# Optimization experiments

Hardware: AMD Instinct MI355X
Metric: run time of the kernel (lower is better)

Reference implementation:

```python
import jax, jax.numpy as jnp
import numpy as np

EPS_LN = 1e-05   # LayerNorm eps in SimpleCogVideoXLayerNormZero
EPS_QK = 1e-06   # RMSNorm eps for qk_norm

DIM = 2048
FFN = 8192
HEADS = 16
HEAD_DIM = DIM // HEADS
TEMB = 512
F, H, W = 4, 24, 24
SEQ = F * H * W  # 2304
B = 1


def _layernorm(x, weight, bias, eps):
    mu = jnp.mean(x, axis=-1, keepdims=True)
    var = jnp.mean((x - mu) ** 2, axis=-1, keepdims=True)
    return (x - mu) * jax.lax.rsqrt(var + eps) * weight + bias


def _rmsnorm(x, weight, eps):
    var = jnp.mean(x * x, axis=-1, keepdims=True)
    return x * jax.lax.rsqrt(var + eps) * weight


def _ln_zero(x, temb, lin_w, lin_b, n_w, n_b):
    # shift/scale/gate modulation from temb
    t = jax.nn.silu(temb) @ lin_w + lin_b          # [B, 3*dim]
    shift, scale, gate = jnp.split(t, 3, axis=1)
    xn = _layernorm(x, n_w, n_b, EPS_LN)
    return xn * (1.0 + scale)[:, None, :] + shift[:, None, :], gate[:, None, :]


def _rope(x, cos, sin):
    # x: [B, S, H, D]; cos/sin: [S, 1, D] broadcastable
    x1 = x[..., 0::2]
    x2 = x[..., 1::2]
    c = cos[..., 0::2]
    s = sin[..., 1::2]
    even = x1 * c - x2 * s
    odd = x1 * s + x2 * c
    return jnp.stack([even, odd], axis=-1).reshape(x.shape)


def _forward(hidden_states, ref_states, temb, cos_h, sin_h, cos_r, sin_r,
             ln1_lw, ln1_lb, ln1_nw, ln1_nb, ln2_lw, ln2_lb, ln2_nw, ln2_nb,
             wq, bq, wk, bk, wv, bv, nq_w, nk_w, wo, bo,
             ffn_w1, ffn_b1, ffn_w2, ffn_b2, f, h, w):
    b, s, dim = hidden_states.shape
    heads = HEADS
    hd = dim // heads
    scale = hd ** -0.5

    def qkv(x, cos, sin):
        q = _rmsnorm(x @ wq + bq, nq_w, EPS_QK)
        k = _rmsnorm(x @ wk + bk, nk_w, EPS_QK)
        v = x @ wv + bv
        q = q.reshape(b, s, heads, hd)
        k = k.reshape(b, s, heads, hd)
        v = v.reshape(b, s, heads, hd)
        q = _rope(q, cos, sin)
        k = _rope(k, cos, sin)
        return q, k, v

    def attn(nh, nr):
        q, k, v = qkv(nh, cos_h, sin_h)
        rq, rk, rv = qkv(nr, cos_r, sin_r)

        def combine(a, ra):
            a = a.reshape(b, f, h, w, heads, hd)
            ra = ra.reshape(b, f, h, w, heads, hd)
            c = jnp.concatenate([a, ra], axis=3)          # [b,f,h,2w,H,D]
            return c.reshape(b * f, h * 2 * w, heads, hd)  # [(bf),(h 2w),H,D]

        cq, ck, cv = combine(q, rq), combine(k, rk), combine(v, rv)
        logits = jnp.einsum('bqhd,bkhd->bhqk', cq, ck) * scale
        probs = jax.nn.softmax(logits, axis=-1)
        out = jnp.einsum('bhqk,bkhd->bqhd', probs, cv)
        out = out.reshape(b, f, h, 2 * w, heads, hd)
        ah = out[:, :, :, :w].reshape(b, s, dim)
        ar = out[:, :, :, w:].reshape(b, s, dim)
        return ah @ wo + bo, ar @ wo + bo

    def ffn(x):
        return jax.nn.gelu(x @ ffn_w1 + ffn_b1, approximate=True) @ ffn_w2 + ffn_b2

    norm_h, gate_h = _ln_zero(hidden_states, temb, ln1_lw, ln1_lb, ln1_nw, ln1_nb)
    norm_r, gate_r = _ln_zero(ref_states, temb, ln1_lw, ln1_lb, ln1_nw, ln1_nb)
    attn_h, attn_r = attn(norm_h, norm_r)

    hidden_states = hidden_states + gate_h * attn_h
    norm_h2, gate_ff = _ln_zero(hidden_states, temb, ln2_lw, ln2_lb, ln2_nw, ln2_nb)
    ref_states = ref_states + gate_r * attn_r
    norm_r2, gate_ff_r = _ln_zero(ref_states, temb, ln2_lw, ln2_lb, ln2_nw, ln2_nb)

    hidden_states = hidden_states + gate_ff * ffn(norm_h2)
    ref_states = ref_states + gate_ff_r * ffn(norm_r2)
    return hidden_states, ref_states


def setup_inputs() -> dict:
    key = jax.random.key(0)
    ks = jax.random.split(key, 24)
    std = 0.02
    inp = {
        'hidden_states': jax.random.normal(ks[0], (B, SEQ, DIM), jnp.float32),
        'ref_states': jax.random.normal(ks[1], (B, SEQ, DIM), jnp.float32),
        'temb': jax.random.normal(ks[2], (B, TEMB), jnp.float32),
        'cos_h': jax.random.uniform(ks[3], (SEQ, 1, HEAD_DIM), jnp.float32),
        'sin_h': jax.random.uniform(ks[4], (SEQ, 1, HEAD_DIM), jnp.float32),
        'cos_r': jax.random.uniform(ks[5], (SEQ, 1, HEAD_DIM), jnp.float32),
        'sin_r': jax.random.uniform(ks[6], (SEQ, 1, HEAD_DIM), jnp.float32),
        'ln1_lw': jax.random.normal(ks[7], (TEMB, 3 * DIM), jnp.float32) * std,
        'ln1_lb': jnp.zeros((3 * DIM,), jnp.float32),
        'ln1_nw': jnp.ones((DIM,), jnp.float32),
        'ln1_nb': jnp.zeros((DIM,), jnp.float32),
        'ln2_lw': jax.random.normal(ks[8], (TEMB, 3 * DIM), jnp.float32) * std,
        'ln2_lb': jnp.zeros((3 * DIM,), jnp.float32),
        'ln2_nw': jnp.ones((DIM,), jnp.float32),
        'ln2_nb': jnp.zeros((DIM,), jnp.float32),
        'wq': jax.random.normal(ks[9], (DIM, DIM), jnp.float32) * std,
        'bq': jnp.zeros((DIM,), jnp.float32),
        'wk': jax.random.normal(ks[10], (DIM, DIM), jnp.float32) * std,
        'bk': jnp.zeros((DIM,), jnp.float32),
        'wv': jax.random.normal(ks[11], (DIM, DIM), jnp.float32) * std,
        'bv': jnp.zeros((DIM,), jnp.float32),
        'nq_w': jnp.ones((DIM,), jnp.float32),
        'nk_w': jnp.ones((DIM,), jnp.float32),
        'wo': jax.random.normal(ks[12], (DIM, DIM), jnp.float32) * std,
        'bo': jnp.zeros((DIM,), jnp.float32),
        'ffn_w1': jax.random.normal(ks[13], (DIM, FFN), jnp.float32) * std,
        'ffn_b1': jnp.zeros((FFN,), jnp.float32),
        'ffn_w2': jax.random.normal(ks[14], (FFN, DIM), jnp.float32) * std,
        'ffn_b2': jnp.zeros((DIM,), jnp.float32),
        'f': F, 'h': H, 'w': W,
    }
    return inp


def reference(hidden_states, ref_states, temb, cos_h, sin_h, cos_r, sin_r,
              ln1_lw, ln1_lb, ln1_nw, ln1_nb, ln2_lw, ln2_lb, ln2_nw, ln2_nb,
              wq, bq, wk, bk, wv, bv, nq_w, nk_w, wo, bo,
              ffn_w1, ffn_b1, ffn_w2, ffn_b2, f, h, w):
    return _forward(hidden_states, ref_states, temb, cos_h, sin_h, cos_r, sin_r,
                    ln1_lw, ln1_lb, ln1_nw, ln1_nb, ln2_lw, ln2_lb, ln2_nw, ln2_nb,
                    wq, bq, wk, bk, wv, bv, nq_w, nk_w, wo, bo,
                    ffn_w1, ffn_b1, ffn_w2, ffn_b2, f, h, w)
```

## Files before the change

### kernel.cpp

```cpp
#include <hip/hip_runtime.h>

typedef unsigned int u32;
typedef unsigned short us16;
typedef __bf16 bf16x8 __attribute__((ext_vector_type(8)));
typedef float f32x4 __attribute__((ext_vector_type(4)));

constexpr int S    = 2304;
constexpr int S2   = 4608;
constexpr int D    = 2048;
constexpr int NQKV = 3 * D;
constexpr int NH   = 16;
constexpr int HD   = 128;
constexpr int FFN  = 8192;
constexpr int CT   = 1152;
constexpr float ATTN_SCALE = 0.08838834764831845f;

__device__ __forceinline__ us16 f2bf(float f) {
  u32 x = __float_as_uint(f);
  x += 0x7fffu + ((x >> 16) & 1u);
  return (us16)(x >> 16);
}
__device__ __forceinline__ float blk_sum256(float v, float* red, int tid) {
  #pragma unroll
  for (int o = 32; o; o >>= 1) v += __shfl_down(v, o, 64);
  __syncthreads();
  if ((tid & 63) == 0) red[tid >> 6] = v;
  __syncthreads();
  return red[0] + red[1] + red[2] + red[3];
}

typedef const __attribute__((address_space(1))) void* gas_ptr;
typedef __attribute__((address_space(3))) void* las_ptr;
__device__ __forceinline__ void gload16(const us16* g, us16* l) {
  __builtin_amdgcn_global_load_lds((gas_ptr)g, (las_ptr)l, 16, 0, 0);
}

__device__ __forceinline__ float gelu_tanh(float x) {
  float y = 0.7978845608028654f * (x + 0.044715f * x * x * x);
  float e = __expf(2.0f * y);
  float t = 1.0f - 2.0f / (e + 1.0f);
  return 0.5f * x * (1.0f + t);
}

__global__ __launch_bounds__(256) void transpose_cvt(
    const float* __restrict__ in, us16* __restrict__ out, int Kd, int Nd) {
  __shared__ float tile[32][33];
  int tx = threadIdx.x, ty = threadIdx.y;
  int n0 = blockIdx.x * 32, k0 = blockIdx.y * 32;
  #pragma unroll
  for (int i = 0; i < 4; i++)
    tile[ty + i * 8][tx] = in[(size_t)(k0 + ty + i * 8) * Nd + n0 + tx];
  __syncthreads();
  #pragma unroll
  for (int i = 0; i < 4; i++)
    out[(size_t)(n0 + ty + i * 8) * Kd + k0 + tx] = f2bf(tile[tx][ty + i * 8]);
}

__global__ __launch_bounds__(256) void temb_mod(
    const float* __restrict__ temb,
    const float* __restrict__ lw1, const float* __restrict__ lb1,
    const float* __restrict__ lw2, const float* __restrict__ lb2,
    float* __restrict__ t1, float* __restrict__ t2) {
  __shared__ float st[512];
  int tid = threadIdx.x;
  for (int i = tid; i < 512; i += 256) {
    float v = temb[i];
    st[i] = v / (1.0f + __expf(-v));
  }
  __syncthreads();
  int which = blockIdx.x / 24;
  int n = (blockIdx.x % 24) * 256 + tid;
  const float* lw = which ? lw2 : lw1;
  const float* lb = which ? lb2 : lb1;
  float acc = lb[n];
  #pragma unroll 4
  for (int k = 0; k < 512; k++) acc += st[k] * lw[(size_t)k * (3 * D) + n];
  (which ? t2 : t1)[n] = acc;
}

__global__ __launch_bounds__(256) void ln_mod(
    const float* __restrict__ x, const float* __restrict__ t,
    const float* __restrict__ nw, const float* __restrict__ nb,
    us16* __restrict__ out) {
  __shared__ float red[4];
  int tok = blockIdx.x, tid = threadIdx.x;
  const float* xr = x + (size_t)tok * D;
  float v[8];
  float4 a = *(const float4*)(xr + tid * 8);
  float4 b = *(const float4*)(xr + tid * 8 + 4);
  v[0]=a.x; v[1]=a.y; v[2]=a.z; v[3]=a.w; v[4]=b.x; v[5]=b.y; v[6]=b.z; v[7]=b.w;
  float s = 0;
  #pragma unroll
  for (int i = 0; i < 8; i++) s += v[i];
  float mu = blk_sum256(s, red, tid) * (1.0f / D);
  float sq = 0;
  #pragma unroll
  for (int i = 0; i < 8; i++) { float d = v[i] - mu; sq += d * d; }
  float var = blk_sum256(sq, red, tid) * (1.0f / D);
  float rinv = rsqrtf(var + 1e-5f);
  int n = tid * 8;
  us16 o[8];
  #pragma unroll
  for (int i = 0; i < 8; i++) {
    float xn = (v[i] - mu) * rinv * nw[n + i] + nb[n + i];
    float y = xn * (1.0f + t[D + n + i]) + t[n + i];
    o[i] = f2bf(y);
  }
  *(uint4*)(out + (size_t)tok * D + n) = *(uint4*)o;
}

template <int EPI>
__global__ __launch_bounds__(256) void gemm128(
    const us16* __restrict__ A, const us16* __restrict__ BT,
    const float* __restrict__ b0, const float* __restrict__ b1,
    const float* __restrict__ b2, int bmask, void* __restrict__ Cout,
    int M, int N, int K,
    const float* __restrict__ xa, const float* __restrict__ xb,
    const float* __restrict__ gate) {
  __shared__ __align__(16) us16 As[3][128 * 32];
  __shared__ __align__(16) us16 Bs[3][128 * 32];
  const int tid = threadIdx.x;

  const int nbx = N >> 7;
  const int nwg = nbx * (M >> 7);
  int bid = (int)blockIdx.x;
  bid = (bid & 7) * (nwg >> 3) + (bid >> 3);
  const int by = bid / nbx;
  const int m0 = by << 7;
  const int n0 = (bid - by * nbx) << 7;

  const int srow = tid >> 2;
  const int scol = (tid & 3) << 3;
  const us16* Ap = A + (size_t)(m0 + srow) * K + scol;
  const us16* Bp = BT + (size_t)(n0 + srow) * K + scol;
  const size_t rstep = (size_t)64 * K;
  const int wvofs = (tid >> 6) << 9;

  const int w = tid >> 6, l = tid & 63;
  const int wr = (w >> 1) << 6, wc = (w & 1) << 6;
  const int m = l & 15, quad = l >> 4;
  const int aoff = (wr + m) * 32 + quad * 8;
  const int boff = (wc + m) * 32 + quad * 8;

  us16 *p0a = &As[0][0], *p1a = &As[1][0], *p2a = &As[2][0];
  us16 *p0b = &Bs[0][0], *p1b = &Bs[1][0], *p2b = &Bs[2][0];

  gload16(Ap,          p0a + wvofs);
  gload16(Ap + rstep,  p0a + wvofs + 2048);
  gload16(Bp,          p0b + wvofs);
  gload16(Bp + rstep,  p0b + wvofs + 2048);
  gload16(Ap + 32,         p1a + wvofs);
  gload16(Ap + rstep + 32, p1a + wvofs + 2048);
  gload16(Bp + 32,         p1b + wvofs);
  gload16(Bp + rstep + 32, p1b + wvofs + 2048);
  asm volatile("s_waitcnt vmcnt(4)" ::: "memory");
  __builtin_amdgcn_s_barrier();
  __builtin_amdgcn_sched_barrier(0);

  f32x4 acc[4][4] = {};
  for (int k0 = 0; k0 < K; k0 += 32) {
    const int k2 = k0 + 64;
    if (k2 < K) {
      gload16(Ap + k2,         p2a + wvofs);
      gload16(Ap + rstep + k2, p2a + wvofs + 2048);
      gload16(Bp + k2,         p2b + wvofs);
      gload16(Bp + rstep + k2, p2b + wvofs + 2048);
    }
    __builtin_amdgcn_sched_barrier(0);
    bf16x8 af[4], bf[4];
    #pragma unroll
    for (int i = 0; i < 4; i++) {
      af[i] = *(const bf16x8*)(p0a + aoff + i * 512);
      bf[i] = *(const bf16x8*)(p0b + boff + i * 512);
    }
    #pragma unroll
    for (int mi = 0; mi < 4; mi++)
      #pragma unroll
      for (int ni = 0; ni < 4; ni++)
        acc[mi][ni] = __builtin_amdgcn_mfma_f32_16x16x32_bf16(
            af[mi], bf[ni], acc[mi][ni], 0, 0, 0);
    __builtin_amdgcn_sched_barrier(0);
    if (k2 < K) asm volatile("s_waitcnt vmcnt(4)" ::: "memory");
    else        asm volatile("s_waitcnt vmcnt(0)" ::: "memory");
    __builtin_amdgcn_s_barrier();
    __builtin_amdgcn_sched_barrier(0);
    us16* t;
    t = p0a; p0a = p1a; p1a = p2a; p2a = t;
    t = p0b; p0b = p1b; p1b = p2b; p2b = t;
  }

  const float* bp = b0;
  if (b1) { int seg = (n0 + wc) >> 11; if (seg == 1) bp = b1; else if (seg >= 2) bp = b2; }

  const int r0 = m0 + wr + (quad << 2);
  #pragma unroll
  for (int ni = 0; ni < 4; ni++) {
    const int col = n0 + wc + ni * 16 + m;
    const float bv = bp ? bp[col & bmask] : 0.0f;
    #pragma unroll
    for (int mi = 0; mi < 4; mi++) {
      const int row = r0 + mi * 16;
      #pragma unroll
      for (int r = 0; r < 4; r++) {
        float y = acc[mi][ni][r] + bv;
        if constexpr (EPI == 1) {
          ((us16*)Cout)[(size_t)(row + r) * N + col] = f2bf(gelu_tanh(y));
        } else if constexpr (EPI == 2) {
          const int rr = row + r;
          const float xv = (rr < S) ? xa[(size_t)rr * N + col]
                                    : xb[(size_t)(rr - S) * N + col];
          ((float*)Cout)[(size_t)rr * N + col] = xv + gate[col & bmask] * y;
        } else {
          ((float*)Cout)[(size_t)(row + r) * N + col] = y;
        }
      }
    }
  }
}

__global__ __launch_bounds__(256) void qkv_scatter(
    const float* __restrict__ raw,
    const float* __restrict__ nq_w, const float* __restrict__ nk_w,
    const float* __restrict__ cos_h, const float* __restrict__ sin_h,
    const float* __restrict__ cos_r, const float* __restrict__ sin_r,
    us16* __restrict__ qc, us16* __restrict__ kc, us16* __restrict__ vc) {
  __shared__ float red[4];
  int bid = blockIdx.x, tid = threadIdx.x;
  int mode = bid / S2;
  int t = bid - mode * S2;
  us16* out = mode == 0 ? qc : (mode == 1 ? kc : vc);
  const float* nw = mode == 1 ? nk_w : nq_w;
  int is_ref = t >= S;
  int tt = is_ref ? t - S : t;
  const float* xr = raw + (size_t)t * NQKV + mode * D;
  float v[8];
  float4 a = *(const float4*)(xr + tid * 8);
  float4 b = *(const float4*)(xr + tid * 8 + 4);
  v[0]=a.x; v[1]=a.y; v[2]=a.z; v[3]=a.w; v[4]=b.x; v[5]=b.y; v[6]=b.z; v[7]=b.w;
  int n = tid * 8;
  int head = n >> 7, d = n & 127;
  float o8[8];
  if (mode < 2) {
    float s = 0;
    #pragma unroll
    for (int i = 0; i < 8; i++) s += v[i] * v[i];
    float tot = blk_sum256(s, red, tid);
    float rinv = rsqrtf(tot * (1.0f / D) + 1e-6f);
    const float* cr = (is_ref ? cos_r : cos_h) + (size_t)tt * HD;
    const float* sr = (is_ref ? sin_r : sin_h) + (size_t)tt * HD;
    #pragma unroll
    for (int p = 0; p < 4; p++) {
      float x1 = v[2 * p] * rinv * nw[n + 2 * p];
      float x2 = v[2 * p + 1] * rinv * nw[n + 2 * p + 1];
      float ce = cr[d + 2 * p];
      float so = sr[d + 2 * p + 1];
      o8[2 * p]     = x1 * ce - x2 * so;
      o8[2 * p + 1] = x1 * so + x2 * ce;
    }
    if (mode == 0) {
      #pragma unroll
      for (int i = 0; i < 8; i++) o8[i] *= ATTN_SCALE;
    }
  } else {
    #pragma unroll
    for (int i = 0; i < 8; i++) o8[i] = v[i];
  }
  int f = tt / 576, rem = tt % 576;
  int row = rem / 24, col = rem - row * 24;
  int comb = row * 48 + col + (is_ref ? 24 : 0);
  size_t oidx = ((size_t)(f * NH + head) * CT + comb) * HD + d;
  us16 packed[8];
  #pragma unroll
  for (int i = 0; i < 8; i++) packed[i] = f2bf(o8[i]);
  *(uint4*)(out + oidx) = *(uint4*)packed;
}

__global__ __launch_bounds__(256) void attn_mfma(
    const us16* __restrict__ qc, const us16* __restrict__ kc,
    const us16* __restrict__ vc, us16* __restrict__ ah, us16* __restrict__ ar) {
  __shared__ __align__(16) us16 Qs[64][136];
  __shared__ __align__(16) us16 Ks[64][136];
  __shared__ __align__(16) us16 Vts[128][72];
  __shared__ __align__(16) us16 Ps[4][16][72];
  int tid = threadIdx.x;
  int w = tid >> 6, l = tid & 63;
  int m = l & 15, quad = l >> 4;
  int bx = blockIdx.x;
  int fh = bx / 18, qt = bx % 18;
  size_t base = (size_t)fh * CT * HD;
  int qbase = qt * 64;

  {
    int row = tid >> 2, c0 = (tid & 3) * 32;
    const us16* src = qc + base + (size_t)(qbase + row) * HD + c0;
    #pragma unroll
    for (int j = 0; j < 4; j++)
      *(uint4*)&Qs[row][c0 + 8 * j] = *(const uint4*)(src + 8 * j);
  }
  __syncthreads();
  bf16x8 qf[4];
  #pragma unroll
  for (int c = 0; c < 4; c++)
    qf[c] = *(const bf16x8*)&Qs[16 * w + m][32 * c + quad * 8];

  float mo[4] = {-1e30f, -1e30f, -1e30f, -1e30f};
  float li[4] = {0.f, 0.f, 0.f, 0.f};
  f32x4 o[8] = {};

  #pragma unroll 1
  for (int kb = 0; kb < CT; kb += 64) {
    __syncthreads();
    {
      int row = tid >> 2, c0 = (tid & 3) * 32;
      const us16* src = kc + base + (size_t)(kb + row) * HD + c0;
      #pragma unroll
      for (int j = 0; j < 4; j++)
        *(uint4*)&Ks[row][c0 + 8 * j] = *(const uint4*)(src + 8 * j);
    }
    {
      int key = tid & 63, d0 = (tid >> 6) * 32;
      const us16* src = vc + base + (size_t)(kb + key) * HD + d0;
      #pragma unroll
      for (int j = 0; j < 4; j++) {
        uint4 vv = *(const uint4*)(src + 8 * j);
        us16 tmp[8];
        *(uint4*)tmp = vv;
        #pragma unroll
        for (int i = 0; i < 8; i++) Vts[d0 + 8 * j + i][key] = tmp[i];
      }
    }
    __syncthreads();
    f32x4 s[4] = {};
    #pragma unroll
    for (int kt = 0; kt < 4; kt++) {
      #pragma unroll
      for (int c = 0; c < 4; c++) {
        bf16x8 kf = *(const bf16x8*)&Ks[kt * 16 + m][32 * c + quad * 8];
        s[kt] = __builtin_amdgcn_mfma_f32_16x16x32_bf16(qf[c], kf, s[kt], 0, 0, 0);
      }
    }
    float al[4];
    #pragma unroll
    for (int r = 0; r < 4; r++) {
      float v = fmaxf(fmaxf(s[0][r], s[1][r]), fmaxf(s[2][r], s[3][r]));
      #pragma unroll
      for (int off = 8; off; off >>= 1) v = fmaxf(v, __shfl_xor(v, off));
      float mn = fmaxf(mo[r], v);
      al[r] = __expf(mo[r] - mn);
      mo[r] = mn;
      float ps = 0.f;
      #pragma unroll
      for (int kt = 0; kt < 4; kt++) {
        float p = __expf(s[kt][r] - mn);
        s[kt][r] = p;
        ps += p;
      }
      #pragma unroll
      for (int off = 8; off; off >>= 1) ps += __shfl_xor(ps, off);
      li[r] = li[r] * al[r] + ps;
    }
    #pragma unroll
    for (int kt = 0; kt < 4; kt++)
      #pragma unroll
      for (int r = 0; r < 4; r++)
        Ps[w][quad * 4 + r][kt * 16 + m] = f2bf(s[kt][r]);
    #pragma unroll
    for (int dt = 0; dt < 8; dt++)
      #pragma unroll
      for (int r = 0; r < 4; r++)
        o[dt][r] *= al[r];
    __syncthreads();
    #pragma unroll
    for (int c = 0; c < 2; c++) {
      bf16x8 pf = *(const bf16x8*)&Ps[w][m][32 * c + quad * 8];
      #pragma unroll
      for (int dt = 0; dt < 8; dt++) {
        bf16x8 vf = *(const bf16x8*)&Vts[dt * 16 + m][32 * c + quad * 8];
        o[dt] = __builtin_amdgcn_mfma_f32_16x16x32_bf16(pf, vf, o[dt], 0, 0, 0);
      }
    }
  }
  int f = fh >> 4, h = fh & 15;
  #pragma unroll
  for (int r = 0; r < 4; r++) {
    float rl = 1.0f / li[r];
    int q = qbase + 16 * w + quad * 4 + r;
    int row = q / 48, cc = q - row * 48;
    int isr = cc >= 24;
    int tok = f * 576 + row * 24 + (isr ? cc - 24 : cc);
    us16* dstp = (isr ? ar : ah) + (size_t)tok * D + h * HD;
    #pragma unroll
    for (int dt = 0; dt < 8; dt++)
      dstp[dt * 16 + m] = f2bf(o[dt][r] * rl);
  }
}

constexpr size_t O_WQ   = 0;
constexpr size_t O_WK   = 8388608;
constexpr size_t O_WV   = 16777216;
constexpr size_t O_WO   = 25165824;
constexpr size_t O_NHR  = 33603584;
constexpr size_t O_RAW  = 52477952;
constexpr size_t O_QC   = 165724160;
constexpr size_t O_KC   = 184598528;
constexpr size_t O_VC   = 203472896;
constexpr size_t O_T1   = 222347264;
constexpr size_t O_T2   = 222371840;
constexpr size_t O_AH   = O_RAW;
constexpr size_t O_W1T  = 0;
constexpr size_t O_W2T  = 33554432;
constexpr size_t O_N2   = 67108864;
constexpr size_t O_MIDB = 85983232;

extern "C" void kernel_launch(void* const* d_in, const int* in_sizes, int n_in,
                              void* d_out, int out_size, void* d_ws, size_t ws_size,
                              hipStream_t stream) {
  (void)in_sizes; (void)n_in; (void)out_size; (void)ws_size;
  const float* hidden = (const float*)d_in[0];
  const float* refs   = (const float*)d_in[1];
  const float* temb   = (const float*)d_in[2];
  const float* cos_h  = (const float*)d_in[3];
  const float* sin_h  = (const float*)d_in[4];
  const float* cos_r  = (const float*)d_in[5];
  const float* sin_r  = (const float*)d_in[6];
  const float* ln1_lw = (const float*)d_in[7];
  const float* ln1_lb = (const float*)d_in[8];
  const float* ln1_nw = (const float*)d_in[9];
  const float* ln1_nb = (const float*)d_in[10];
  const float* ln2_lw = (const float*)d_in[11];
  const float* ln2_lb = (const float*)d_in[12];
  const float* ln2_nw = (const float*)d_in[13];
  const float* ln2_nb = (const float*)d_in[14];
  const float* wq = (const float*)d_in[15];
  const float* bq = (const float*)d_in[16];
  const float* wk = (const float*)d_in[17];
  const float* bk = (const float*)d_in[18];
  const float* wv = (const float*)d_in[19];
  const float* bv = (const float*)d_in[20];
  const float* nq_w = (const float*)d_in[21];
  const float* nk_w = (const float*)d_in[22];
  const float* wo = (const float*)d_in[23];
  const float* bo = (const float*)d_in[24];
  const float* ffn_w1 = (const float*)d_in[25];
  const float* ffn_b1 = (const float*)d_in[26];
  const float* ffn_w2 = (const float*)d_in[27];
  const float* ffn_b2 = (const float*)d_in[28];

  char* ws = (char*)d_ws;
  us16* p_wq  = (us16*)(ws + O_WQ);
  us16* p_wk  = (us16*)(ws + O_WK);
  us16* p_wv  = (us16*)(ws + O_WV);
  us16* p_wo  = (us16*)(ws + O_WO);
  us16* p_nhr = (us16*)(ws + O_NHR);
  float* p_raw = (float*)(ws + O_RAW);
  us16* p_qc  = (us16*)(ws + O_QC);
  us16* p_kc  = (us16*)(ws + O_KC);
  us16* p_vc  = (us16*)(ws + O_VC);
  float* p_t1 = (float*)(ws + O_T1);
  float* p_t2 = (float*)(ws + O_T2);
  us16* p_ah  = (us16*)(ws + O_AH);
  us16* p_ar  = p_ah + (size_t)S * D;
  us16* p_w1t = (us16*)(ws + O_W1T);
  us16* p_w2t = (us16*)(ws + O_W2T);
  us16* p_n2  = (us16*)(ws + O_N2);
  us16* p_midb = (us16*)(ws + O_MIDB);
  float* outd = (float*)d_out;

  constexpr int G_QKV  = (NQKV / 128) * (S2 / 128);
  constexpr int G_WO   = (D / 128) * (S2 / 128);
  constexpr int G_FFN1 = (FFN / 128) * (S2 / 128);
  constexpr int G_FFN2 = G_WO;

  dim3 tb(32, 8);
  transpose_cvt<<<dim3(64, 64), tb, 0, stream>>>(wq, p_wq, D, D);
  transpose_cvt<<<dim3(64, 64), tb, 0, stream>>>(wk, p_wk, D, D);
  transpose_cvt<<<dim3(64, 64), tb, 0, stream>>>(wv, p_wv, D, D);
  transpose_cvt<<<dim3(64, 64), tb, 0, stream>>>(wo, p_wo, D, D);
  temb_mod<<<48, 256, 0, stream>>>(temb, ln1_lw, ln1_lb, ln2_lw, ln2_lb, p_t1, p_t2);
  ln_mod<<<S, 256, 0, stream>>>(hidden, p_t1, ln1_nw, ln1_nb, p_nhr);
  ln_mod<<<S, 256, 0, stream>>>(refs,   p_t1, ln1_nw, ln1_nb, p_nhr + (size_t)S * D);
  gemm128<0><<<G_QKV, 256, 0, stream>>>(p_nhr, p_wq, bq, bk, bv, D - 1,
                                        p_raw, S2, NQKV, D,
                                        nullptr, nullptr, nullptr);
  qkv_scatter<<<3 * S2, 256, 0, stream>>>(p_raw, nq_w, nk_w,
                                          cos_h, sin_h, cos_r, sin_r,
                                          p_qc, p_kc, p_vc);
  attn_mfma<<<64 * 18, 256, 0, stream>>>(p_qc, p_kc, p_vc, p_ah, p_ar);
  gemm128<2><<<G_WO, 256, 0, stream>>>(p_ah, p_wo, bo, nullptr, nullptr, D - 1,
                                       outd, S2, D, D,
                                       hidden, refs, p_t1 + 2 * D);
  transpose_cvt<<<dim3(256, 64), tb, 0, stream>>>(ffn_w1, p_w1t, D, FFN);
  transpose_cvt<<<dim3(64, 256), tb, 0, stream>>>(ffn_w2, p_w2t, FFN, D);
  ln_mod<<<S2, 256, 0, stream>>>(outd, p_t2, ln2_nw, ln2_nb, p_n2);
  gemm128<1><<<G_FFN1, 256, 0, stream>>>(p_n2, p_w1t, ffn_b1, nullptr, nullptr,
                                         FFN - 1, p_midb, S2, FFN, D,
                                         nullptr, nullptr, nullptr);
  gemm128<2><<<G_FFN2, 256, 0, stream>>>(p_midb, p_w2t, ffn_b2, nullptr, nullptr,
                                         D - 1, outd, S2, D, FFN,
                                         outd, outd + (size_t)S * D, p_t2 + 2 * D);
}
```

Baseline: 1.471 ms.

## Replace triple-buffered GEMM pipeline with single-buffer loop and add 128x256 wide-tile GEMM

The three-stage LDS prefetch pipeline in gemm128 becomes a simple single-buffered loop that synchronises before and after each k-step load. A new 512-thread gemmW kernel with 128x256 tiles is added and used for the QKV and FFN1 projections, doubling B-tile reuse per workgroup. The simpler loop lowers LDS use and may raise occupancy, but it gives up the overlap of global loads with MFMA work.

```diff
diff --git a/kernel.cpp b/kernel.cpp
--- a/kernel.cpp
+++ b/kernel.cpp
@@ -117,8 +117,8 @@
     int M, int N, int K,
     const float* __restrict__ xa, const float* __restrict__ xb,
     const float* __restrict__ gate) {
-  __shared__ __align__(16) us16 As[3][128 * 32];
-  __shared__ __align__(16) us16 Bs[3][128 * 32];
+  __shared__ __align__(16) us16 As[128 * 32];
+  __shared__ __align__(16) us16 Bs[128 * 32];
   const int tid = threadIdx.x;
 
   const int nbx = N >> 7;
@@ -134,44 +134,28 @@
   const us16* Ap = A + (size_t)(m0 + srow) * K + scol;
   const us16* Bp = BT + (size_t)(n0 + srow) * K + scol;
   const size_t rstep = (size_t)64 * K;
-  const int wvofs = (tid >> 6) << 9;
+  us16* lA = As + ((tid >> 6) << 9);
+  us16* lB = Bs + ((tid >> 6) << 9);
 
   const int w = tid >> 6, l = tid & 63;
   const int wr = (w >> 1) << 6, wc = (w & 1) << 6;
   const int m = l & 15, quad = l >> 4;
-  const int aoff = (wr + m) * 32 + quad * 8;
-  const int boff = (wc + m) * 32 + quad * 8;
-
-  us16 *p0a = &As[0][0], *p1a = &As[1][0], *p2a = &As[2][0];
-  us16 *p0b = &Bs[0][0], *p1b = &Bs[1][0], *p2b = &Bs[2][0];
-
-  gload16(Ap,          p0a + wvofs);
-  gload16(Ap + rstep,  p0a + wvofs + 2048);
-  gload16(Bp,          p0b + wvofs);
-  gload16(Bp + rstep,  p0b + wvofs + 2048);
-  gload16(Ap + 32,         p1a + wvofs);
-  gload16(Ap + rstep + 32, p1a + wvofs + 2048);
-  gload16(Bp + 32,         p1b + wvofs);
-  gload16(Bp + rstep + 32, p1b + wvofs + 2048);
-  asm volatile("s_waitcnt vmcnt(4)" ::: "memory");
-  __builtin_amdgcn_s_barrier();
-  __builtin_amdgcn_sched_barrier(0);
+  const us16* Ard = As + (wr + m) * 32 + quad * 8;
+  const us16* Brd = Bs + (wc + m) * 32 + quad * 8;
 
   f32x4 acc[4][4] = {};
   for (int k0 = 0; k0 < K; k0 += 32) {
-    const int k2 = k0 + 64;
-    if (k2 < K) {
-      gload16(Ap + k2,         p2a + wvofs);
-      gload16(Ap + rstep + k2, p2a + wvofs + 2048);
-      gload16(Bp + k2,         p2b + wvofs);
-      gload16(Bp + rstep + k2, p2b + wvofs + 2048);
-    }
-    __builtin_amdgcn_sched_barrier(0);
+    __syncthreads();
+    gload16(Ap + k0, lA);
+    gload16(Ap + rstep + k0, lA + 2048);
+    gload16(Bp + k0, lB);
+    gload16(Bp + rstep + k0, lB + 2048);
+    __syncthreads();
     bf16x8 af[4], bf[4];
     #pragma unroll
     for (int i = 0; i < 4; i++) {
-      af[i] = *(const bf16x8*)(p0a + aoff + i * 512);
-      bf[i] = *(const bf16x8*)(p0b + boff + i * 512);
+      af[i] = *(const bf16x8*)(Ard + i * 512);
+      bf[i] = *(const bf16x8*)(Brd + i * 512);
     }
     #pragma unroll
     for (int mi = 0; mi < 4; mi++)
@@ -179,14 +163,6 @@
       for (int ni = 0; ni < 4; ni++)
         acc[mi][ni] = __builtin_amdgcn_mfma_f32_16x16x32_bf16(
             af[mi], bf[ni], acc[mi][ni], 0, 0, 0);
-    __builtin_amdgcn_sched_barrier(0);
-    if (k2 < K) asm volatile("s_waitcnt vmcnt(4)" ::: "memory");
-    else        asm volatile("s_waitcnt vmcnt(0)" ::: "memory");
-    __builtin_amdgcn_s_barrier();
-    __builtin_amdgcn_sched_barrier(0);
-    us16* t;
-    t = p0a; p0a = p1a; p1a = p2a; p2a = t;
-    t = p0b; p0b = p1b; p1b = p2b; p2b = t;
   }
 
   const float* bp = b0;
@@ -210,6 +186,85 @@
           const float xv = (rr < S) ? xa[(size_t)rr * N + col]
                                     : xb[(size_t)(rr - S) * N + col];
           ((float*)Cout)[(size_t)rr * N + col] = xv + gate[col & bmask] * y;
+        } else {
+          ((float*)Cout)[(size_t)(row + r) * N + col] = y;
+        }
+      }
+    }
+  }
+}
+
+template <int EPI>
+__global__ __launch_bounds__(512) void gemmW(
+    const us16* __restrict__ A, const us16* __restrict__ BT,
+    const float* __restrict__ b0, const float* __restrict__ b1,
+    const float* __restrict__ b2, int bmask, void* __restrict__ Cout,
+    int M, int N, int K) {
+  __shared__ __align__(16) us16 As[128 * 32];
+  __shared__ __align__(16) us16 Bs[256 * 32];
+  const int tid = threadIdx.x;
+
+  const int nbx = N >> 8;
+  const int nwg = nbx * (M >> 7);
+  int bid = (int)blockIdx.x;
+  bid = (bid & 7) * (nwg >> 3) + (bid >> 3);
+  const int by = bid / nbx;
+  const int m0 = by << 7;
+  const int n0 = (bid - by * nbx) << 8;
+
+  const int srow = tid >> 2;
+  const int scol = (tid & 3) << 3;
+  const us16* Ap  = A  + (size_t)(m0 + srow) * K + scol;
+  const us16* Bp  = BT + (size_t)(n0 + srow) * K + scol;
+  const us16* Bp2 = BT + (size_t)(n0 + 128 + srow) * K + scol;
+  const int w = tid >> 6;
+  us16* lA = As + (w << 9);
+  us16* lB = Bs + (w << 9);
+
+  const int l = tid & 63;
+  const int wr = (w >> 2) << 6;
+  const int wc = (w & 3) << 6;
+  const int m = l & 15, quad = l >> 4;
+  const us16* Ard = As + (wr + m) * 32 + quad * 8;
+  const us16* Brd = Bs + (wc + m) * 32 + quad * 8;
+
+  f32x4 acc[4][4] = {};
+  for (int k0 = 0; k0 < K; k0 += 32) {
+    __syncthreads();
+    gload16(Ap + k0,  lA);
+    gload16(Bp + k0,  lB);
+    gload16(Bp2 + k0, lB + 4096);
+    __syncthreads();
+    bf16x8 af[4], bf[4];
+    #pragma unroll
+    for (int i = 0; i < 4; i++) {
+      af[i] = *(const bf16x8*)(Ard + i * 512);
+      bf[i] = *(const bf16x8*)(Brd + i * 512);
+    }
+    #pragma unroll
+    for (int mi = 0; mi < 4; mi++)
+      #pragma unroll
+      for (int ni = 0; ni < 4; ni++)
+        acc[mi][ni] = __builtin_amdgcn_mfma_f32_16x16x32_bf16(
+            af[mi], bf[ni], acc[mi][ni], 0, 0, 0);
+  }
+
+  const float* bp = b0;
+  if (b1) { int seg = (n0 + wc) >> 11; if (seg == 1) bp = b1; else if (seg >= 2) bp = b2; }
+
+  const int r0 = m0 + wr + (quad << 2);
+  #pragma unroll
+  for (int ni = 0; ni < 4; ni++) {
+    const int col = n0 + wc + ni * 16 + m;
+    const float bv = bp ? bp[col & bmask] : 0.0f;
+    #pragma unroll
+    for (int mi = 0; mi < 4; mi++) {
+      const int row = r0 + mi * 16;
+      #pragma unroll
+      for (int r = 0; r < 4; r++) {
+        float y = acc[mi][ni][r] + bv;
+        if constexpr (EPI == 1) {
+          ((us16*)Cout)[(size_t)(row + r) * N + col] = f2bf(gelu_tanh(y));
         } else {
           ((float*)Cout)[(size_t)(row + r) * N + col] = y;
         }
@@ -466,9 +521,9 @@
   us16* p_midb = (us16*)(ws + O_MIDB);
   float* outd = (float*)d_out;
 
-  constexpr int G_QKV  = (NQKV / 128) * (S2 / 128);
+  constexpr int G_QKV  = (NQKV / 256) * (S2 / 128);
   constexpr int G_WO   = (D / 128) * (S2 / 128);
-  constexpr int G_FFN1 = (FFN / 128) * (S2 / 128);
+  constexpr int G_FFN1 = (FFN / 256) * (S2 / 128);
   constexpr int G_FFN2 = G_WO;
 
   dim3 tb(32, 8);
@@ -479,9 +534,8 @@
   temb_mod<<<48, 256, 0, stream>>>(temb, ln1_lw, ln1_lb, ln2_lw, ln2_lb, p_t1, p_t2);
   ln_mod<<<S, 256, 0, stream>>>(hidden, p_t1, ln1_nw, ln1_nb, p_nhr);
   ln_mod<<<S, 256, 0, stream>>>(refs,   p_t1, ln1_nw, ln1_nb, p_nhr + (size_t)S * D);
-  gemm128<0><<<G_QKV, 256, 0, stream>>>(p_nhr, p_wq, bq, bk, bv, D - 1,
-                                        p_raw, S2, NQKV, D,
-                                        nullptr, nullptr, nullptr);
+  gemmW<0><<<G_QKV, 512, 0, stream>>>(p_nhr, p_wq, bq, bk, bv, D - 1,
+                                      p_raw, S2, NQKV, D);
   qkv_scatter<<<3 * S2, 256, 0, stream>>>(p_raw, nq_w, nk_w,
                                           cos_h, sin_h, cos_r, sin_r,
                                           p_qc, p_kc, p_vc);
@@ -492,9 +546,8 @@
   transpose_cvt<<<dim3(256, 64), tb, 0, stream>>>(ffn_w1, p_w1t, D, FFN);
   transpose_cvt<<<dim3(64, 256), tb, 0, stream>>>(ffn_w2, p_w2t, FFN, D);
   ln_mod<<<S2, 256, 0, stream>>>(outd, p_t2, ln2_nw, ln2_nb, p_n2);
-  gemm128<1><<<G_FFN1, 256, 0, stream>>>(p_n2, p_w1t, ffn_b1, nullptr, nullptr,
-                                         FFN - 1, p_midb, S2, FFN, D,
-                                         nullptr, nullptr, nullptr);
+  gemmW<1><<<G_FFN1, 512, 0, stream>>>(p_n2, p_w1t, ffn_b1, nullptr, nullptr,
+                                       FFN - 1, p_midb, S2, FFN, D);
   gemm128<2><<<G_FFN2, 256, 0, stream>>>(p_midb, p_w2t, ffn_b2, nullptr, nullptr,
                                          D - 1, outd, S2, D, FFN,
                                          outd, outd + (size_t)S * D, p_t2 + 2 * D);
```

Measured after the change: 1.495 ms. No clear change (+1.7%).
